# Performance work log

Measured on AMD Instinct MI355X. Metric: run time of the kernel, lower is better.

## Reference

```python
import jax, jax.numpy as jnp
import numpy as np

KEY_SIZE = 512


def setup_inputs() -> dict:
    key = jax.random.key(0)
    ks = jax.random.split(key, 4)
    B, T, C = 8, 2048, 512
    s = 0.02
    return {
        "x": jax.random.normal(ks[0], (B, T, C), dtype=jnp.float32),
        "Wq": jax.random.normal(ks[1], (KEY_SIZE, C), dtype=jnp.float32) * s,
        "bq": jnp.zeros((KEY_SIZE,), dtype=jnp.float32),
        "Wk": jax.random.normal(ks[2], (KEY_SIZE, C), dtype=jnp.float32) * s,
        "bk": jnp.zeros((KEY_SIZE,), dtype=jnp.float32),
        "Wv": jax.random.normal(ks[3], (KEY_SIZE, C), dtype=jnp.float32) * s,
        "bv": jnp.zeros((KEY_SIZE,), dtype=jnp.float32),
    }


def reference(x, Wq, bq, Wk, bk, Wv, bv):
    # x: [B, T, C]; Linear(y) = y @ W.T + b (torch convention)
    q = jnp.einsum("btc,kc->btk", x, Wq) + bq  # [B, T, K]
    k = jnp.einsum("btc,kc->btk", x, Wk) + bk  # [B, T, K]
    v = jnp.einsum("btc,vc->btv", x, Wv) + bv  # [B, T, V]

    scores = jnp.einsum("bqk,bsk->bqs", q, k)  # [B, Tq, Tk]
    T = x.shape[1]
    # mask[j, i] = 1 if i > j  -> strict upper triangle masked with -inf
    mask = jnp.triu(jnp.ones((T, T), dtype=bool), k=1)
    scores = jnp.where(mask[None, :, :], -jnp.inf, scores)
    # NOTE: original divides by sqrt(key_size) AFTER masking, and takes
    # softmax over dim=1 (the QUERY axis) — faithfully reproduced.
    probs = jax.nn.softmax(scores / jnp.sqrt(jnp.asarray(KEY_SIZE, scores.dtype)), axis=1)
    attn = jnp.einsum("bqs,bsv->bqv", probs, v)  # [B, T, V]
    return jnp.concatenate([x, attn], axis=2)  # [B, T, C + V]
```

## Files before the change

### kernel.cpp

```cpp
#include <hip/hip_runtime.h>

#define BATCH 8
#define TSEQ  2048
#define CDIM  512
#define MTOK  (BATCH*TSEQ)
#define NTRI  136

typedef __attribute__((ext_vector_type(8))) short bf16x8;
typedef __attribute__((ext_vector_type(4))) float f32x4;

__device__ __forceinline__ unsigned short f2bf(float f) {
    union { float f; unsigned int u; } v; v.f = f;
    unsigned int r = v.u + 0x7FFF + ((v.u >> 16) & 1);
    return (unsigned short)(r >> 16);
}
__device__ __forceinline__ float bfl(unsigned short u) {
    union { unsigned int i; float f; } v; v.i = ((unsigned int)u) << 16; return v.f;
}

__device__ __forceinline__ f32x4 fzero() { f32x4 z = {0.f, 0.f, 0.f, 0.f}; return z; }

__device__ __forceinline__ void gl2lds16(const void* g, void* l) {
    __builtin_amdgcn_global_load_lds(
        (const __attribute__((address_space(1))) unsigned int*)g,
        (__attribute__((address_space(3))) unsigned int*)l, 16, 0, 0);
}

__device__ __forceinline__ void stage_tile(const unsigned short* src, size_t ld,
                                           unsigned short* buf, int t) {
    const unsigned short* s0 = src + (size_t)(t >> 2) * ld + (t & 3) * 8;
    gl2lds16(s0, &buf[t * 8]);
    gl2lds16(s0 + (size_t)64 * ld, &buf[2048 + t * 8]);
}

__global__ __launch_bounds__(256) void k_convert_x(const float* __restrict__ x,
                                                   unsigned short* __restrict__ xb,
                                                   float* __restrict__ out) {
    int i = blockIdx.x * blockDim.x + threadIdx.x;
    float4 v = ((const float4*)x)[i];
    ushort4 o;
    o.x = f2bf(v.x); o.y = f2bf(v.y); o.z = f2bf(v.z); o.w = f2bf(v.w);
    ((ushort4*)xb)[i] = o;
    int e = i * 4;
    int row = e >> 9;
    int c   = e & 511;
    *(float4*)(out + (size_t)row * 1024 + c) = v;
}

__global__ __launch_bounds__(256) void k_convert_w(const float* __restrict__ w,
                                                   unsigned short* __restrict__ wb) {
    int i = blockIdx.x * blockDim.x + threadIdx.x;
    float4 v = ((const float4*)w)[i];
    ushort4 o;
    o.x = f2bf(v.x); o.y = f2bf(v.y); o.z = f2bf(v.z); o.w = f2bf(v.w);
    ((ushort4*)wb)[i] = o;
}

__global__ __launch_bounds__(256) void k_qkv(const unsigned short* __restrict__ xb,
                                             const unsigned short* __restrict__ Wcat,
                                             const float* __restrict__ bq,
                                             const float* __restrict__ bk,
                                             const float* __restrict__ bv,
                                             unsigned short* __restrict__ QKb,
                                             unsigned short* __restrict__ Vt) {
    __shared__ __align__(16) unsigned short lds[18432];
    int orig = blockIdx.x;
    int flat = (orig & 7) * 192 + (orig >> 3);
    int mt = flat / 12, nt = flat - mt * 12;
    int m0 = mt * 128, n0 = nt * 128;
    int t = threadIdx.x, w = t >> 6, lane = t & 63, quad = lane >> 4, lane16 = lane & 15;
    int rowHalf = (w >> 1) * 64, colHalf = (w & 1) * 64;

    const unsigned short* Arows = xb + (size_t)m0 * 512;
    const unsigned short* Brows = Wcat + (size_t)n0 * 512;

    f32x4 acc[4][4];
#pragma unroll
    for (int i = 0; i < 4; i++)
#pragma unroll
        for (int j = 0; j < 4; j++) acc[i][j] = fzero();

    stage_tile(Arows, 512, lds, t);
    stage_tile(Brows, 512, lds + 4096, t);
    __syncthreads();
    int cur = 0;
    for (int k0 = 0; k0 < CDIM; k0 += 32) {
        unsigned short* As = lds + cur * 8192;
        unsigned short* Bs = As + 4096;
        if (k0 + 32 < CDIM) {
            unsigned short* An = lds + (cur ^ 1) * 8192;
            stage_tile(Arows + k0 + 32, 512, An, t);
            stage_tile(Brows + k0 + 32, 512, An + 4096, t);
        }
        bf16x8 a[4], b[4];
#pragma unroll
        for (int mi = 0; mi < 4; mi++)
            a[mi] = *(const bf16x8*)&As[(rowHalf + mi * 16 + lane16) * 32 + quad * 8];
#pragma unroll
        for (int ni = 0; ni < 4; ni++)
            b[ni] = *(const bf16x8*)&Bs[(colHalf + ni * 16 + lane16) * 32 + quad * 8];
#pragma unroll
        for (int mi = 0; mi < 4; mi++)
#pragma unroll
            for (int ni = 0; ni < 4; ni++)
                acc[mi][ni] = __builtin_amdgcn_mfma_f32_16x16x32_bf16(a[mi], b[ni], acc[mi][ni], 0, 0, 0);
        __syncthreads();
        cur ^= 1;
    }

    int which = n0 >> 9;
    if (which < 2) {
        const float* bias = which ? bk : bq;
        unsigned short* T = &lds[w * 4608];
#pragma unroll
        for (int ni = 0; ni < 4; ni++) {
            int n = (n0 & 511) + colHalf + ni * 16 + lane16;
            float bb = bias[n];
#pragma unroll
            for (int mi = 0; mi < 4; mi++)
#pragma unroll
                for (int r = 0; r < 4; r++)
                    T[(mi * 16 + quad * 4 + r) * 72 + ni * 16 + lane16] =
                        f2bf(acc[mi][ni][r] + bb);
        }
        int colBase = which * 512 + (n0 & 511) + colHalf;
#pragma unroll
        for (int i = 0; i < 8; i++) {
            int rl = i * 8 + (lane >> 3);
            int cl = (lane & 7) * 8;
            int m = m0 + rowHalf + rl;
            *(uint4*)(QKb + (size_t)m * 1024 + colBase + cl) = *(const uint4*)&T[rl * 72 + cl];
        }
    } else {
        unsigned short* T = &lds[w * 2048];
        int b = m0 >> 11, tbase = (m0 & 2047) + rowHalf;
#pragma unroll
        for (int p = 0; p < 2; p++) {
            __syncthreads();
#pragma unroll
            for (int j = 0; j < 2; j++) {
                int ni = p * 2 + j;
                int n = (n0 & 511) + colHalf + ni * 16 + lane16;
                float bb = bv[n];
                int vl = j * 16 + lane16;
#pragma unroll
                for (int mi = 0; mi < 4; mi++)
#pragma unroll
                    for (int r = 0; r < 4; r++)
                        T[vl * 64 + mi * 16 + quad * 4 + r] = f2bf(acc[mi][ni][r] + bb);
            }
            __syncthreads();
#pragma unroll
            for (int i = 0; i < 4; i++) {
                int vl = i * 8 + (lane >> 3);
                int tl = (lane & 7) * 8;
                int v = (n0 & 511) + colHalf + p * 32 + vl;
                *(uint4*)(Vt + ((size_t)(b * 512 + v)) * 2048 + tbase + tl) =
                    *(const uint4*)&T[vl * 64 + tl];
            }
        }
    }
}

__global__ __launch_bounds__(256) void k_score(const unsigned short* __restrict__ QKb,
                                               unsigned short* __restrict__ Pbuf,
                                               float* __restrict__ colsum) {
    __shared__ __align__(16) unsigned short lds[16384];
    int orig = blockIdx.x;
    int bb  = orig & 7;
    int idx = orig >> 3;
    int qt = (int)((sqrtf(8.0f * idx + 1.0f) - 1.0f) * 0.5f);
    while ((qt + 1) * (qt + 2) / 2 <= idx) qt++;
    while (qt * (qt + 1) / 2 > idx) qt--;
    int st = idx - qt * (qt + 1) / 2;
    int q0 = qt * 128, s0 = st * 128;

    int t = threadIdx.x, w = t >> 6, lane = t & 63, quad = lane >> 4, lane16 = lane & 15;
    int rowHalf = (w >> 1) * 64, colHalf = (w & 1) * 64;
    const unsigned short* Qrows = QKb + ((size_t)(bb * 2048 + q0)) * 1024;
    const unsigned short* Krows = QKb + ((size_t)(bb * 2048 + s0)) * 1024 + 512;

    f32x4 acc[4][4];
#pragma unroll
    for (int i = 0; i < 4; i++)
#pragma unroll
        for (int j = 0; j < 4; j++) acc[i][j] = fzero();

    stage_tile(Qrows, 1024, lds, t);
    stage_tile(Krows, 1024, lds + 4096, t);
    __syncthreads();
    int cur = 0;
    for (int k0 = 0; k0 < CDIM; k0 += 32) {
        unsigned short* As = lds + cur * 8192;
        unsigned short* Bs = As + 4096;
        if (k0 + 32 < CDIM) {
            unsigned short* An = lds + (cur ^ 1) * 8192;
            stage_tile(Qrows + k0 + 32, 1024, An, t);
            stage_tile(Krows + k0 + 32, 1024, An + 4096, t);
        }
        bf16x8 a[4], b[4];
#pragma unroll
        for (int mi = 0; mi < 4; mi++)
            a[mi] = *(const bf16x8*)&As[(rowHalf + mi * 16 + lane16) * 32 + quad * 8];
#pragma unroll
        for (int ni = 0; ni < 4; ni++)
            b[ni] = *(const bf16x8*)&Bs[(colHalf + ni * 16 + lane16) * 32 + quad * 8];
#pragma unroll
        for (int mi = 0; mi < 4; mi++)
#pragma unroll
            for (int ni = 0; ni < 4; ni++)
                acc[mi][ni] = __builtin_amdgcn_mfma_f32_16x16x32_bf16(a[mi], b[ni], acc[mi][ni], 0, 0, 0);
        __syncthreads();
        cur ^= 1;
    }

    const float scale = 0.044194173824159216f;
    unsigned short* T = &lds[w * 4096];
    float csum[4] = {0.f, 0.f, 0.f, 0.f};
#pragma unroll
    for (int ni = 0; ni < 4; ni++) {
        int s = s0 + colHalf + ni * 16 + lane16;
#pragma unroll
        for (int mi = 0; mi < 4; mi++)
#pragma unroll
            for (int r = 0; r < 4; r++) {
                int q = q0 + rowHalf + mi * 16 + quad * 4 + r;
                float p = 0.0f;
                if (s <= q) { p = __expf(acc[mi][ni][r] * scale); csum[ni] += p; }
                T[(mi * 16 + quad * 4 + r) * 64 + ni * 16 + lane16] = f2bf(p);
            }
    }
#pragma unroll
    for (int ni = 0; ni < 4; ni++) {
        float v = csum[ni];
        v += __shfl_xor(v, 16);
        v += __shfl_xor(v, 32);
        if (quad == 0)
            unsafeAtomicAdd(&colsum[bb * 2048 + s0 + colHalf + ni * 16 + lane16], v);
    }
    __syncthreads();
    unsigned short* tile = Pbuf + ((size_t)(bb * NTRI + idx)) * 16384;
#pragma unroll
    for (int i = 0; i < 8; i++) {
        int rl = i * 8 + (lane >> 3);
        int cl = (lane & 7) * 8;
        *(uint4*)(tile + (rowHalf + rl) * 128 + colHalf + cl) = *(const uint4*)&T[rl * 64 + cl];
    }
}

__global__ __launch_bounds__(256) void k_invcs(float* __restrict__ cs) {
    int i = blockIdx.x * 256 + threadIdx.x;
    cs[i] = 1.0f / cs[i];
}

__global__ __launch_bounds__(256) void k_vscale(unsigned short* __restrict__ Vt,
                                                const float* __restrict__ inv) {
    int idx = blockIdx.x * 256 + threadIdx.x;
    int s8  = idx & 255;
    int row = idx >> 8;
    int b   = row >> 9;
    uint4 raw = ((const uint4*)Vt)[idx];
    const float* ip = inv + b * TSEQ + s8 * 8;
    unsigned int rr[4] = {raw.x, raw.y, raw.z, raw.w};
    unsigned int oo[4];
#pragma unroll
    for (int j = 0; j < 4; j++) {
        float f0 = bfl((unsigned short)(rr[j] & 0xffff)) * ip[j * 2];
        float f1 = bfl((unsigned short)(rr[j] >> 16))    * ip[j * 2 + 1];
        oo[j] = (unsigned int)f2bf(f0) | ((unsigned int)f2bf(f1) << 16);
    }
    uint4 o = {oo[0], oo[1], oo[2], oo[3]};
    ((uint4*)Vt)[idx] = o;
}

__global__ __launch_bounds__(256) void k_attn(const unsigned short* __restrict__ Pbuf,
                                              const unsigned short* __restrict__ Vt,
                                              float* __restrict__ out) {
    __shared__ __align__(16) unsigned short lds[16384];
    int i = blockIdx.x;
    int slot = i & 255, half = i >> 8;
    int qt = half ? (15 - (slot >> 5)) : (slot >> 5);
    int bv = slot & 31;
    int bb = bv >> 2;
    int v0 = (bv & 3) * 128;
    int t = threadIdx.x, w = t >> 6, lane = t & 63, quad = lane >> 4, lane16 = lane & 15;
    int rowHalf = (w >> 1) * 64, colHalf = (w & 1) * 64;

    const unsigned short* Pb = Pbuf + ((size_t)(bb * NTRI + qt * (qt + 1) / 2)) * 16384;
    const unsigned short* Vb = Vt + ((size_t)(bb * 512 + v0)) * 2048;

    f32x4 acc[4][4];
#pragma unroll
    for (int ii = 0; ii < 4; ii++)
#pragma unroll
        for (int j = 0; j < 4; j++) acc[ii][j] = fzero();

    int Kend = (qt + 1) * 128;
    stage_tile(Pb, 128, lds, t);
    stage_tile(Vb, 2048, lds + 4096, t);
    __syncthreads();
    int cur = 0;
    for (int k0 = 0; k0 < Kend; k0 += 32) {
        unsigned short* As = lds + cur * 8192;
        unsigned short* Bs = As + 4096;
        int k1 = k0 + 32;
        if (k1 < Kend) {
            unsigned short* An = lds + (cur ^ 1) * 8192;
            stage_tile(Pb + (size_t)(k1 >> 7) * 16384 + (k1 & 127), 128, An, t);
            stage_tile(Vb + k1, 2048, An + 4096, t);
        }
        bf16x8 a[4], b[4];
#pragma unroll
        for (int mi = 0; mi < 4; mi++)
            a[mi] = *(const bf16x8*)&As[(rowHalf + mi * 16 + lane16) * 32 + quad * 8];
#pragma unroll
        for (int ni = 0; ni < 4; ni++)
            b[ni] = *(const bf16x8*)&Bs[(colHalf + ni * 16 + lane16) * 32 + quad * 8];
#pragma unroll
        for (int mi = 0; mi < 4; mi++)
#pragma unroll
            for (int ni = 0; ni < 4; ni++)
                acc[mi][ni] = __builtin_amdgcn_mfma_f32_16x16x32_bf16(a[mi], b[ni], acc[mi][ni], 0, 0, 0);
        __syncthreads();
        cur ^= 1;
    }

#pragma unroll
    for (int mi = 0; mi < 4; mi++)
#pragma unroll
        for (int ni = 0; ni < 4; ni++)
#pragma unroll
            for (int r = 0; r < 4; r++) {
                int q = qt * 128 + rowHalf + mi * 16 + quad * 4 + r;
                int v = v0 + colHalf + ni * 16 + lane16;
                out[((size_t)(bb * 2048 + q)) * 1024 + 512 + v] = acc[mi][ni][r];
            }
}

extern "C" void kernel_launch(void* const* d_in, const int* in_sizes, int n_in,
                              void* d_out, int out_size, void* d_ws, size_t ws_size,
                              hipStream_t stream) {
    const float* x  = (const float*)d_in[0];
    const float* Wq = (const float*)d_in[1];
    const float* bq = (const float*)d_in[2];
    const float* Wk = (const float*)d_in[3];
    const float* bk = (const float*)d_in[4];
    const float* Wv = (const float*)d_in[5];
    const float* bv = (const float*)d_in[6];
    float* out = (float*)d_out;

    char* ws = (char*)d_ws;
    size_t off = 0;
    auto alloc = [&](size_t bytes) -> void* {
        void* p = ws + off;
        off += (bytes + 255) & ~(size_t)255;
        return p;
    };
    unsigned short* QKb = (unsigned short*)alloc((size_t)MTOK * 1024 * 2);
    unsigned short* Vt  = (unsigned short*)alloc((size_t)MTOK * CDIM * 2);
    float* colsum = (float*)alloc((size_t)BATCH * TSEQ * 4);
    size_t mark = off;
    unsigned short* Wcat = (unsigned short*)alloc((size_t)3 * CDIM * CDIM * 2);
    unsigned short* xb   = (unsigned short*)alloc((size_t)MTOK * CDIM * 2);
    unsigned short* Pbuf = (unsigned short*)(ws + mark);
    (void)ws_size;

    k_convert_x<<<(MTOK * CDIM / 4) / 256, 256, 0, stream>>>(x, xb, out);
    k_convert_w<<<(CDIM * CDIM / 4) / 256, 256, 0, stream>>>(Wq, Wcat);
    k_convert_w<<<(CDIM * CDIM / 4) / 256, 256, 0, stream>>>(Wk, Wcat + (size_t)CDIM * CDIM);
    k_convert_w<<<(CDIM * CDIM / 4) / 256, 256, 0, stream>>>(Wv, Wcat + (size_t)2 * CDIM * CDIM);

    k_qkv<<<1536, 256, 0, stream>>>(xb, Wcat, bq, bk, bv, QKb, Vt);

    hipMemsetAsync(colsum, 0, (size_t)BATCH * TSEQ * 4, stream);
    k_score<<<1088, 256, 0, stream>>>(QKb, Pbuf, colsum);

    k_invcs<<<(BATCH * TSEQ) / 256, 256, 0, stream>>>(colsum);
    k_vscale<<<(MTOK * CDIM / 8) / 256, 256, 0, stream>>>(Vt, colsum);

    k_attn<<<512, 256, 0, stream>>>(Pbuf, Vt, out);
}
```

Baseline: 223.4 us.

## Enlarge QKV GEMM tiles to 256x256 with swizzled LDS and merge weight conversions

Rewrites the QKV projection GEMM to use 256x256 output tiles with 512 threads, a K-step of 64, XOR-swizzled LDS staging to avoid bank conflicts, and setprio around the MFMA bursts. The three weight-conversion launches are merged into one kernel. The larger tiles raise data reuse per LDS load and cut the number of blocks and launches. In exchange they raise register and LDS pressure: 128 KB of LDS per block and 128 accumulators per thread, which may lower occupancy.

```diff
diff --git a/kernel.cpp b/kernel.cpp
--- a/kernel.cpp
+++ b/kernel.cpp
@@ -47,116 +47,151 @@
     *(float4*)(out + (size_t)row * 1024 + c) = v;
 }
 
-__global__ __launch_bounds__(256) void k_convert_w(const float* __restrict__ w,
-                                                   unsigned short* __restrict__ wb) {
-    int i = blockIdx.x * blockDim.x + threadIdx.x;
-    float4 v = ((const float4*)w)[i];
+__global__ __launch_bounds__(256) void k_convert_w3(const float* __restrict__ Wq,
+                                                    const float* __restrict__ Wk,
+                                                    const float* __restrict__ Wv,
+                                                    unsigned short* __restrict__ wb) {
+    int i = blockIdx.x * 256 + threadIdx.x;
+    int m = i >> 16;
+    const float* w = (m == 0) ? Wq : ((m == 1) ? Wk : Wv);
+    float4 v = ((const float4*)w)[i & 65535];
     ushort4 o;
     o.x = f2bf(v.x); o.y = f2bf(v.y); o.z = f2bf(v.z); o.w = f2bf(v.w);
     ((ushort4*)wb)[i] = o;
 }
 
-__global__ __launch_bounds__(256) void k_qkv(const unsigned short* __restrict__ xb,
-                                             const unsigned short* __restrict__ Wcat,
-                                             const float* __restrict__ bq,
-                                             const float* __restrict__ bk,
-                                             const float* __restrict__ bv,
-                                             unsigned short* __restrict__ QKb,
-                                             unsigned short* __restrict__ Vt) {
-    __shared__ __align__(16) unsigned short lds[18432];
+__global__ __launch_bounds__(512, 2) void k_qkv(const unsigned short* __restrict__ xb,
+                                                const unsigned short* __restrict__ Wcat,
+                                                const float* __restrict__ bq,
+                                                const float* __restrict__ bk,
+                                                const float* __restrict__ bv,
+                                                unsigned short* __restrict__ QKb,
+                                                unsigned short* __restrict__ Vt) {
+    __shared__ __align__(16) unsigned short lds[65536];
     int orig = blockIdx.x;
-    int flat = (orig & 7) * 192 + (orig >> 3);
-    int mt = flat / 12, nt = flat - mt * 12;
-    int m0 = mt * 128, n0 = nt * 128;
-    int t = threadIdx.x, w = t >> 6, lane = t & 63, quad = lane >> 4, lane16 = lane & 15;
-    int rowHalf = (w >> 1) * 64, colHalf = (w & 1) * 64;
-
-    const unsigned short* Arows = xb + (size_t)m0 * 512;
-    const unsigned short* Brows = Wcat + (size_t)n0 * 512;
-
-    f32x4 acc[4][4];
-#pragma unroll
-    for (int i = 0; i < 4; i++)
+    int flat = (orig & 7) * 48 + (orig >> 3);
+    int mt = flat / 6, nt = flat - mt * 6;
+    int m0 = mt * 256, n0 = nt * 256;
+    int t = threadIdx.x, w = t >> 6, lane = t & 63;
+    int quad = lane >> 4, lane16 = lane & 15;
+    int wr = w >> 2, wc = w & 3;
+    int l3 = lane >> 3;
+    int sl = (lane & 7) ^ l3;
+    int rswz = (lane16 & 7) << 3;
+
+    const unsigned short* Abase = xb + (size_t)m0 * 512;
+    const unsigned short* Bbase = Wcat + (size_t)n0 * 512;
+
+    f32x4 acc[8][4];
+#pragma unroll
+    for (int i = 0; i < 8; i++)
 #pragma unroll
         for (int j = 0; j < 4; j++) acc[i][j] = fzero();
 
-    stage_tile(Arows, 512, lds, t);
-    stage_tile(Brows, 512, lds + 4096, t);
+    auto stage = [&](const unsigned short* src, unsigned short* buf) {
+#pragma unroll
+        for (int i = 0; i < 4; ++i) {
+            int q = i * 8 + w;
+            gl2lds16(src + (size_t)(q * 8 + l3) * 512 + sl * 8,
+                     &buf[q * 512 + lane * 8]);
+        }
+    };
+
+    stage(Abase, &lds[0]);
+    stage(Bbase, &lds[16384]);
     __syncthreads();
-    int cur = 0;
-    for (int k0 = 0; k0 < CDIM; k0 += 32) {
-        unsigned short* As = lds + cur * 8192;
-        unsigned short* Bs = As + 4096;
-        if (k0 + 32 < CDIM) {
-            unsigned short* An = lds + (cur ^ 1) * 8192;
-            stage_tile(Arows + k0 + 32, 512, An, t);
-            stage_tile(Brows + k0 + 32, 512, An + 4096, t);
-        }
-        bf16x8 a[4], b[4];
-#pragma unroll
-        for (int mi = 0; mi < 4; mi++)
-            a[mi] = *(const bf16x8*)&As[(rowHalf + mi * 16 + lane16) * 32 + quad * 8];
-#pragma unroll
-        for (int ni = 0; ni < 4; ni++)
-            b[ni] = *(const bf16x8*)&Bs[(colHalf + ni * 16 + lane16) * 32 + quad * 8];
-#pragma unroll
-        for (int mi = 0; mi < 4; mi++)
-#pragma unroll
-            for (int ni = 0; ni < 4; ni++)
-                acc[mi][ni] = __builtin_amdgcn_mfma_f32_16x16x32_bf16(a[mi], b[ni], acc[mi][ni], 0, 0, 0);
+
+#pragma unroll
+    for (int kt = 0; kt < 8; ++kt) {
+        int c = kt & 1;
+        if (kt + 1 < 8) {
+            stage(Abase + (kt + 1) * 64, &lds[(c ^ 1) * 32768]);
+            stage(Bbase + (kt + 1) * 64, &lds[(c ^ 1) * 32768 + 16384]);
+        }
+        const unsigned short* As = &lds[c * 32768];
+        const unsigned short* Bs = As + 16384;
+
+        bf16x8 bfr[4][2];
+#pragma unroll
+        for (int ni = 0; ni < 4; ++ni) {
+            int row = wc * 64 + ni * 16 + lane16;
+#pragma unroll
+            for (int ks = 0; ks < 2; ++ks)
+                bfr[ni][ks] = *(const bf16x8*)&Bs[row * 64 + ((ks * 32 + quad * 8) ^ rswz)];
+        }
+#pragma unroll
+        for (int mh = 0; mh < 2; ++mh) {
+            bf16x8 afr[4][2];
+#pragma unroll
+            for (int mi2 = 0; mi2 < 4; ++mi2) {
+                int row = wr * 128 + mh * 64 + mi2 * 16 + lane16;
+#pragma unroll
+                for (int ks = 0; ks < 2; ++ks)
+                    afr[mi2][ks] = *(const bf16x8*)&As[row * 64 + ((ks * 32 + quad * 8) ^ rswz)];
+            }
+            __builtin_amdgcn_s_setprio(1);
+#pragma unroll
+            for (int mi2 = 0; mi2 < 4; ++mi2)
+#pragma unroll
+                for (int ni = 0; ni < 4; ++ni)
+#pragma unroll
+                    for (int ks = 0; ks < 2; ++ks)
+                        acc[mh * 4 + mi2][ni] = __builtin_amdgcn_mfma_f32_16x16x32_bf16(
+                            afr[mi2][ks], bfr[ni][ks], acc[mh * 4 + mi2][ni], 0, 0, 0);
+            __builtin_amdgcn_s_setprio(0);
+        }
         __syncthreads();
-        cur ^= 1;
     }
 
     int which = n0 >> 9;
     if (which < 2) {
         const float* bias = which ? bk : bq;
         unsigned short* T = &lds[w * 4608];
-#pragma unroll
-        for (int ni = 0; ni < 4; ni++) {
-            int n = (n0 & 511) + colHalf + ni * 16 + lane16;
-            float bb = bias[n];
-#pragma unroll
-            for (int mi = 0; mi < 4; mi++)
-#pragma unroll
-                for (int r = 0; r < 4; r++)
-                    T[(mi * 16 + quad * 4 + r) * 72 + ni * 16 + lane16] =
-                        f2bf(acc[mi][ni][r] + bb);
-        }
-        int colBase = which * 512 + (n0 & 511) + colHalf;
-#pragma unroll
-        for (int i = 0; i < 8; i++) {
-            int rl = i * 8 + (lane >> 3);
-            int cl = (lane & 7) * 8;
-            int m = m0 + rowHalf + rl;
-            *(uint4*)(QKb + (size_t)m * 1024 + colBase + cl) = *(const uint4*)&T[rl * 72 + cl];
+        int colBase = which * 512 + (n0 & 511) + wc * 64;
+#pragma unroll
+        for (int p = 0; p < 2; ++p) {
+#pragma unroll
+            for (int ni = 0; ni < 4; ++ni) {
+                float bb = bias[(n0 & 511) + wc * 64 + ni * 16 + lane16];
+#pragma unroll
+                for (int mi2 = 0; mi2 < 4; ++mi2)
+#pragma unroll
+                    for (int r = 0; r < 4; ++r)
+                        T[(mi2 * 16 + quad * 4 + r) * 72 + ni * 16 + lane16] =
+                            f2bf(acc[p * 4 + mi2][ni][r] + bb);
+            }
+#pragma unroll
+            for (int i = 0; i < 8; ++i) {
+                int rl = i * 8 + l3;
+                int cl = (lane & 7) * 8;
+                int m = m0 + wr * 128 + p * 64 + rl;
+                *(uint4*)(QKb + (size_t)m * 1024 + colBase + cl) = *(const uint4*)&T[rl * 72 + cl];
+            }
         }
     } else {
-        unsigned short* T = &lds[w * 2048];
-        int b = m0 >> 11, tbase = (m0 & 2047) + rowHalf;
-#pragma unroll
-        for (int p = 0; p < 2; p++) {
-            __syncthreads();
-#pragma unroll
-            for (int j = 0; j < 2; j++) {
+        unsigned short* T = &lds[w * 4352];
+        int b = m0 >> 11, tbase = (m0 & 2047) + wr * 128;
+        int nv = (n0 & 511) + wc * 64;
+#pragma unroll
+        for (int p = 0; p < 2; ++p) {
+#pragma unroll
+            for (int j = 0; j < 2; ++j) {
                 int ni = p * 2 + j;
-                int n = (n0 & 511) + colHalf + ni * 16 + lane16;
-                float bb = bv[n];
+                float bb = bv[nv + ni * 16 + lane16];
                 int vl = j * 16 + lane16;
 #pragma unroll
-                for (int mi = 0; mi < 4; mi++)
-#pragma unroll
-                    for (int r = 0; r < 4; r++)
-                        T[vl * 64 + mi * 16 + quad * 4 + r] = f2bf(acc[mi][ni][r] + bb);
-            }
-            __syncthreads();
-#pragma unroll
-            for (int i = 0; i < 4; i++) {
-                int vl = i * 8 + (lane >> 3);
-                int tl = (lane & 7) * 8;
-                int v = (n0 & 511) + colHalf + p * 32 + vl;
+                for (int mi = 0; mi < 8; ++mi)
+#pragma unroll
+                    for (int r = 0; r < 4; ++r)
+                        T[vl * 136 + mi * 16 + quad * 4 + r] = f2bf(acc[mi][ni][r] + bb);
+            }
+#pragma unroll
+            for (int i = 0; i < 8; ++i) {
+                int vl = i * 4 + quad;
+                int tl = lane16 * 8;
+                int v = nv + p * 32 + vl;
                 *(uint4*)(Vt + ((size_t)(b * 512 + v)) * 2048 + tbase + tl) =
-                    *(const uint4*)&T[vl * 64 + tl];
+                    *(const uint4*)&T[vl * 136 + tl];
             }
         }
     }
@@ -366,11 +401,9 @@
     (void)ws_size;
 
     k_convert_x<<<(MTOK * CDIM / 4) / 256, 256, 0, stream>>>(x, xb, out);
-    k_convert_w<<<(CDIM * CDIM / 4) / 256, 256, 0, stream>>>(Wq, Wcat);
-    k_convert_w<<<(CDIM * CDIM / 4) / 256, 256, 0, stream>>>(Wk, Wcat + (size_t)CDIM * CDIM);
-    k_convert_w<<<(CDIM * CDIM / 4) / 256, 256, 0, stream>>>(Wv, Wcat + (size_t)2 * CDIM * CDIM);
-
-    k_qkv<<<1536, 256, 0, stream>>>(xb, Wcat, bq, bk, bv, QKb, Vt);
+    k_convert_w3<<<(3 * CDIM * CDIM / 4) / 256, 256, 0, stream>>>(Wq, Wk, Wv, Wcat);
+
+    k_qkv<<<384, 512, 0, stream>>>(xb, Wcat, bq, bk, bv, QKb, Vt);
 
     hipMemsetAsync(colsum, 0, (size_t)BATCH * TSEQ * 4, stream);
     k_score<<<1088, 256, 0, stream>>>(QKb, Pbuf, colsum);
```

New measurement: 217.3 us. -2.7%, faster.
